# Optimization experiments

Measured on AMD Instinct MI355X. Metric: run time of the kernel, lower is better.

Reference implementation:

```python
import jax, jax.numpy as jnp
import numpy as np

N = 20000          # nodes
E = 320000         # edges
IN_C = 512         # input features
HID = 512          # 2*out_channels (first GCN layer width)
OUT = 256          # out_channels == num_hidden
PROJ = 256         # num_proj_hidden


def _gcn_conv(x, W, b, src, dst):
    """PyG GCNConv: x' = D^{-1/2}(A+I)D^{-1/2} X W + b (self-loops added)."""
    n = x.shape[0]
    x = x @ W  # [N, F_out]
    ones = jnp.ones((src.shape[0],), x.dtype)
    deg = jax.ops.segment_sum(ones, dst, num_segments=n) + 1.0  # +1 self-loop
    dis = jax.lax.rsqrt(deg)
    coef = dis[src] * dis[dst]                      # [E]
    agg = jax.ops.segment_sum(x[src] * coef[:, None], dst, num_segments=n)
    agg = agg + x * (dis * dis)[:, None]            # self-loop messages
    return agg + b


def setup_inputs() -> dict:
    key = jax.random.key(0)
    ks = jax.random.split(key, 12)
    s = 0.02
    return {
        "node_features": jax.random.normal(ks[0], (N, IN_C), jnp.float32),
        "edge_index": jax.random.randint(ks[1], (2, E), 0, N, jnp.int64),
        "W1": jax.random.normal(ks[2], (IN_C, HID), jnp.float32) * s,
        "b1": jnp.zeros((HID,), jnp.float32),
        "W2": jax.random.normal(ks[3], (HID, OUT), jnp.float32) * s,
        "b2": jnp.zeros((OUT,), jnp.float32),
        "a": jnp.asarray(0.25, jnp.float32),  # shared PReLU weight
        "W3": jax.random.normal(ks[4], (OUT, PROJ), jnp.float32) * s,
        "b3": jnp.zeros((PROJ,), jnp.float32),
        "W4": jax.random.normal(ks[5], (PROJ, OUT), jnp.float32) * s,
        "b4": jnp.zeros((OUT,), jnp.float32),
    }


def reference(node_features, edge_index, W1, b1, W2, b2, a, W3, b3, W4, b4):
    src, dst = edge_index[0], edge_index[1]
    prelu = lambda x: jnp.where(x > 0, x, a * x)
    h = prelu(_gcn_conv(node_features, W1, b1, src, dst))
    h = prelu(_gcn_conv(h, W2, b2, src, dst))
    # projection MLP: Linear -> ELU -> Linear
    h2 = jax.nn.elu(h @ W3 + b3)
    return h2 @ W4 + b4
```

## Files before the change

kernel.cpp:

```cpp
#include <hip/hip_runtime.h>

typedef unsigned short u16;
typedef unsigned int   u32;
typedef __attribute__((ext_vector_type(8))) short short8;
typedef __attribute__((ext_vector_type(4))) float f32x4;

__device__ __forceinline__ float bf2f(u16 h){
    return __uint_as_float(((u32)h) << 16);
}
__device__ __forceinline__ u16 f2bf(float f){
    u32 u = __float_as_uint(f);
    u += 0x7fffu + ((u >> 16) & 1u);
    return (u16)(u >> 16);
}

__global__ void probe_all(const u16* __restrict__ w1, const int* __restrict__ ei,
                          const void* b1, const void* b2, const void* b3,
                          const void* b4, const void* av,
                          int* __restrict__ f32f, int* __restrict__ efmt,
                          int* __restrict__ zf,
                          u16* d1, u16* d2, u16* d3, u16* d4, u16* da){
    __shared__ int sf32, sfmt;
    int t = threadIdx.x;
    if (t == 0){ sf32 = 0; sfmt = 0; }
    __syncthreads();
    {
        int huge = 0;
        #pragma unroll
        for (int k = 0; k < 16; k++){
            u16 h = w1[t * 16 + k];
            if (((h >> 7) & 0xFF) >= 0x7F) huge = 1;
        }
        if (huge) atomicOr(&sf32, 1);
    }
    if (ei[2*t + 1] != 0) atomicOr(&sfmt, 1);
    __syncthreads();
    int f32 = sf32, fmt = sfmt;
    if (t == 0){ f32f[0] = f32; efmt[0] = fmt; zf[0] = 0; }
    #define CV(s,i) (f32 ? f2bf(((const float*)(s))[i]) : ((const u16*)(s))[i])
    d1[t]       = CV(b1, t);
    d1[t + 256] = CV(b1, t + 256);
    d2[t] = CV(b2, t);
    d3[t] = CV(b3, t);
    d4[t] = CV(b4, t);
    if (t == 0) da[0] = CV(av, 0);
    #undef CV
}

__device__ __forceinline__ int eload(const int* ei, int fmt, int idx){
    return fmt ? ei[idx] : ei[2*idx];
}

__global__ void deg_count(const int* __restrict__ ei, const int* __restrict__ efmt,
                          int* __restrict__ cnt, int E, int N){
    int e = blockIdx.x * 256 + threadIdx.x;
    if (e < E){
        int d = eload(ei, efmt[0], E + e);
        if ((unsigned)d < (unsigned)N) atomicAdd(&cnt[d], 1);
    }
}

__global__ void scan1(const int* __restrict__ cnt, int* __restrict__ incl,
                      int* __restrict__ bsum, int N){
    __shared__ int s[256];
    int t = threadIdx.x, i = blockIdx.x * 256 + t;
    int v = (i < N) ? cnt[i] : 0;
    s[t] = v;
    __syncthreads();
    #pragma unroll
    for (int off = 1; off < 256; off <<= 1){
        int u = (t >= off) ? s[t - off] : 0;
        __syncthreads();
        s[t] += u;
        __syncthreads();
    }
    if (i < N) incl[i] = s[t];
    if (t == 255) bsum[blockIdx.x] = s[255];
}

__global__ void scan2(const int* __restrict__ bsum, int* __restrict__ boff,
                      int nb, int* __restrict__ rowstart_last){
    __shared__ int s[128];
    int t = threadIdx.x;
    int v = (t < nb) ? bsum[t] : 0;
    s[t] = v;
    __syncthreads();
    #pragma unroll
    for (int off = 1; off < 128; off <<= 1){
        int u = (t >= off) ? s[t - off] : 0;
        __syncthreads();
        s[t] += u;
        __syncthreads();
    }
    if (t < nb) boff[t] = s[t] - v;
    if (t == nb - 1) rowstart_last[0] = s[t];
}

__global__ void scan3(const int* __restrict__ cnt, const int* __restrict__ incl,
                      const int* __restrict__ boff, int* __restrict__ rowstart,
                      int* __restrict__ cursor, float* __restrict__ dis, int N){
    int i = blockIdx.x * 256 + threadIdx.x;
    if (i < N){
        int v = cnt[i];
        int rsv = boff[blockIdx.x] + incl[i] - v;
        rowstart[i] = rsv;
        cursor[i]   = rsv;
        dis[i] = rsqrtf((float)v + 1.0f);
    }
}

__global__ void csr_fill(const int* __restrict__ ei, const int* __restrict__ efmt,
                         int* __restrict__ cursor, int* __restrict__ csr_src,
                         int E, int N){
    int e = blockIdx.x * 256 + threadIdx.x;
    if (e < E){
        int fmt = efmt[0];
        int d = eload(ei, fmt, E + e);
        if ((unsigned)d < (unsigned)N){
            int p = atomicAdd(&cursor[d], 1);
            csr_src[p] = eload(ei, fmt, e);
        }
    }
}

__global__ void transpose_cvt(const void* __restrict__ in, const int* __restrict__ flag,
                              u16* __restrict__ out, int K, int N){
    __shared__ u16 t[32][33];
    int bx = blockIdx.x * 32;
    int by = blockIdx.y * 32;
    int x = threadIdx.x, y = threadIdx.y;
    int f32 = flag[0];
    #pragma unroll
    for (int i = 0; i < 32; i += 8){
        size_t idx = (size_t)(by + y + i) * N + bx + x;
        t[y + i][x] = f32 ? f2bf(((const float*)in)[idx]) : ((const u16*)in)[idx];
    }
    __syncthreads();
    #pragma unroll
    for (int i = 0; i < 32; i += 8)
        out[(size_t)(bx + y + i) * K + by + x] = t[x][y + i];
}

#define TM 64
#define TN 128
#define BK 32
#define BKP 40

template<int MODE, int OUTF>
__global__ __launch_bounds__(256) void gemm_mfma(
    const void* __restrict__ A, const int* __restrict__ af32,
    const u16* __restrict__ BT,
    const u16* __restrict__ bias, void* __restrict__ Cv,
    int M, int K, int N)
{
    __shared__ __align__(16) u16 As[TM * BKP];
    __shared__ __align__(16) u16 Bs[TN * BKP];
    int tid  = threadIdx.x;
    int lane = tid & 63;
    int wave = tid >> 6;
    int waveM = wave >> 1, waveN = wave & 1;
    int bm = blockIdx.x * TM;
    int bn = blockIdx.y * TN;
    int f32 = af32[0];

    f32x4 acc[2][4] = {};

    int alr = tid >> 2;
    int alc = (tid & 3) * 8;
    int blr = tid >> 1;
    int blc = (tid & 1) * 16;

    for (int k0 = 0; k0 < K; k0 += BK){
        {
            int gr = bm + alr;
            short8 v = {0,0,0,0,0,0,0,0};
            if (gr < M){
                if (f32){
                    const float* p = (const float*)A + (size_t)gr * K + k0 + alc;
                    f32x4 a0 = *(const f32x4*)p;
                    f32x4 a1 = *(const f32x4*)(p + 4);
                    #pragma unroll
                    for (int j = 0; j < 4; j++){
                        v[j]   = (short)f2bf(a0[j]);
                        v[4+j] = (short)f2bf(a1[j]);
                    }
                } else {
                    v = *(const short8*)((const u16*)A + (size_t)gr * K + k0 + alc);
                }
            }
            *(short8*)&As[alr * BKP + alc] = v;
        }
        {
            const u16* p = BT + (size_t)(bn + blr) * K + k0 + blc;
            short8 v0 = *(const short8*)p;
            short8 v1 = *(const short8*)(p + 8);
            *(short8*)&Bs[blr * BKP + blc]     = v0;
            *(short8*)&Bs[blr * BKP + blc + 8] = v1;
        }
        __syncthreads();
        int q = lane >> 4;
        int r16 = lane & 15;
        short8 af[2], bfr[4];
        #pragma unroll
        for (int i = 0; i < 2; i++)
            af[i]  = *(const short8*)&As[(waveM*32 + i*16 + r16) * BKP + q*8];
        #pragma unroll
        for (int j = 0; j < 4; j++)
            bfr[j] = *(const short8*)&Bs[(waveN*64 + j*16 + r16) * BKP + q*8];
        #pragma unroll
        for (int i = 0; i < 2; i++)
            #pragma unroll
            for (int j = 0; j < 4; j++)
                acc[i][j] = __builtin_amdgcn_mfma_f32_16x16x32_bf16(af[i], bfr[j], acc[i][j], 0, 0, 0);
        __syncthreads();
    }

    int q = lane >> 4;
    int c16 = lane & 15;
    #pragma unroll
    for (int i = 0; i < 2; i++){
        #pragma unroll
        for (int j = 0; j < 4; j++){
            int gcol = bn + waveN*64 + j*16 + c16;
            float bvv = (MODE >= 1) ? bf2f(bias[gcol]) : 0.f;
            #pragma unroll
            for (int r = 0; r < 4; r++){
                int grow = bm + waveM*32 + i*16 + q*4 + r;
                if (grow < M){
                    float v = acc[i][j][r] + bvv;
                    if (MODE == 2) v = (v > 0.f) ? v : expm1f(v);
                    if (OUTF) ((float*)Cv)[(size_t)grow * N + gcol] = v;
                    else      ((u16*)Cv)[(size_t)grow * N + gcol] = f2bf(v);
                }
            }
        }
    }
}

template<int F, int NPB>
__global__ __launch_bounds__(F/8*NPB) void aggregate(
    const u16* __restrict__ XW, const int* __restrict__ rowstart,
    const int* __restrict__ csr_src, const float* __restrict__ dis,
    const u16* __restrict__ bias, const u16* __restrict__ aptr,
    u16* __restrict__ out, int N)
{
    int node = blockIdx.x * NPB + threadIdx.y;
    if (node >= N) return;
    int tf = threadIdx.x * 8;
    float a  = bf2f(aptr[0]);
    float di = dis[node];
    int e0 = rowstart[node], e1 = rowstart[node + 1];
    float acc[8] = {0,0,0,0,0,0,0,0};
    int e = e0;
    for (; e + 8 <= e1; e += 8){
        int   si[8];
        float ci[8];
        short8 vi[8];
        #pragma unroll
        for (int u = 0; u < 8; u++) si[u] = csr_src[e + u];
        #pragma unroll
        for (int u = 0; u < 8; u++) ci[u] = dis[si[u]];
        #pragma unroll
        for (int u = 0; u < 8; u++)
            vi[u] = *(const short8*)(XW + (size_t)si[u] * F + tf);
        #pragma unroll
        for (int u = 0; u < 8; u++)
            #pragma unroll
            for (int j = 0; j < 8; j++)
                acc[j] += ci[u] * bf2f((u16)vi[u][j]);
    }
    for (; e + 4 <= e1; e += 4){
        int s0 = csr_src[e], s1 = csr_src[e+1], s2 = csr_src[e+2], s3 = csr_src[e+3];
        float c0 = dis[s0], c1 = dis[s1], c2 = dis[s2], c3 = dis[s3];
        short8 v0 = *(const short8*)(XW + (size_t)s0 * F + tf);
        short8 v1 = *(const short8*)(XW + (size_t)s1 * F + tf);
        short8 v2 = *(const short8*)(XW + (size_t)s2 * F + tf);
        short8 v3 = *(const short8*)(XW + (size_t)s3 * F + tf);
        #pragma unroll
        for (int j = 0; j < 8; j++)
            acc[j] += c0*bf2f((u16)v0[j]) + c1*bf2f((u16)v1[j])
                    + c2*bf2f((u16)v2[j]) + c3*bf2f((u16)v3[j]);
    }
    for (; e < e1; e++){
        int s = csr_src[e];
        float c = dis[s];
        short8 v = *(const short8*)(XW + (size_t)s * F + tf);
        #pragma unroll
        for (int j = 0; j < 8; j++) acc[j] += c * bf2f((u16)v[j]);
    }
    {
        short8 v = *(const short8*)(XW + (size_t)node * F + tf);
        #pragma unroll
        for (int j = 0; j < 8; j++) acc[j] += di * bf2f((u16)v[j]);
    }
    short8 bv = *(const short8*)(bias + tf);
    short8 o;
    #pragma unroll
    for (int j = 0; j < 8; j++){
        float x = di * acc[j] + bf2f((u16)bv[j]);
        x = (x > 0.f) ? x : a * x;
        o[j] = (short)f2bf(x);
    }
    *(short8*)(out + (size_t)node * F + tf) = o;
}

extern "C" void kernel_launch(void* const* d_in, const int* in_sizes, int n_in,
                              void* d_out, int out_size, void* d_ws, size_t ws_size,
                              hipStream_t stream)
{
    int iX=0, iEI=1, iW1=2, ib1=3, iW2=4, ib2=5, ia=6, iW3=7, ib3=8, iW4=9, ib4=10;
    {
        int jX=-1,jEI=-1,jW1=-1,jb1=-1,jW2=-1,ja=-1,jW3=-1,jW4=-1,jb2=-1,jb3=-1,jb4=-1;
        int n64k=0, n256=0;
        for (int i = 0; i < n_in; i++){
            switch (in_sizes[i]){
                case 10240000: jX = i; break;
                case 640000:   jEI = i; break;
                case 262144:   jW1 = i; break;
                case 131072:   jW2 = i; break;
                case 512:      jb1 = i; break;
                case 1:        ja = i; break;
                case 65536:    if (n64k++ == 0) jW3 = i; else jW4 = i; break;
                case 256: {
                    int k = n256++;
                    if (k == 0) jb2 = i; else if (k == 1) jb3 = i; else jb4 = i;
                } break;
                default: break;
            }
        }
        if (jX>=0&&jEI>=0&&jW1>=0&&jb1>=0&&jW2>=0&&ja>=0&&jW3>=0&&jW4>=0&&jb2>=0&&jb3>=0&&jb4>=0){
            iX=jX; iEI=jEI; iW1=jW1; ib1=jb1; iW2=jW2; ib2=jb2; ia=ja; iW3=jW3; ib3=jb3; iW4=jW4; ib4=jb4;
        }
    }
    int N = in_sizes[iX] / 512;
    int E = in_sizes[iEI] / 2;
    const int* EI = (const int*)d_in[iEI];
    float* OUT = (float*)d_out;
    u16*   S   = (u16*)d_out;

    char* ws = (char*)d_ws;
    size_t off = 0;
    auto alloc = [&](size_t bytes)->char*{
        char* p = ws + off;
        off = (off + bytes + 255) & ~(size_t)255;
        return p;
    };
    int nb = (N + 255) / 256;
    int*   cnt  = (int*)  alloc((size_t)N*4);
    int*   incl = (int*)  alloc((size_t)N*4);
    int*   bsum = (int*)  alloc(512);
    int*   boff = (int*)  alloc(512);
    int*   efmt = (int*)  alloc(4);
    int*   f32f = (int*)  alloc(4);
    int*   zf   = (int*)  alloc(4);
    float* dis  = (float*)alloc((size_t)N*4);
    int*   rs   = (int*)  alloc((size_t)(N+1)*4);
    int*   cur  = (int*)  alloc((size_t)N*4);
    int*   csr  = (int*)  alloc((size_t)E*4);
    u16*   WT1  = (u16*)  alloc((size_t)512*512*2);
    u16*   WT2  = (u16*)  alloc((size_t)256*512*2);
    u16*   WT3  = (u16*)  alloc((size_t)256*256*2);
    u16*   WT4  = (u16*)  alloc((size_t)256*256*2);
    u16*   b1c  = (u16*)  alloc((size_t)512*2);
    u16*   b2c  = (u16*)  alloc((size_t)256*2);
    u16*   b3c  = (u16*)  alloc((size_t)256*2);
    u16*   b4c  = (u16*)  alloc((size_t)256*2);
    u16*   ac   = (u16*)  alloc((size_t)8*2);
    u16*   h1   = (u16*)  alloc((size_t)N*512*2);
    u16*   P    = (u16*)  alloc((size_t)N*256*2);

    if (ws_size < off) return;

    hipMemsetAsync(cnt, 0, (size_t)N*4, stream);
    probe_all<<<1, 256, 0, stream>>>((const u16*)d_in[iW1], EI,
                                     d_in[ib1], d_in[ib2], d_in[ib3], d_in[ib4],
                                     d_in[ia], f32f, efmt, zf,
                                     b1c, b2c, b3c, b4c, ac);

    int egrid = (E + 255) / 256;
    deg_count<<<egrid, 256, 0, stream>>>(EI, efmt, cnt, E, N);
    scan1<<<nb, 256, 0, stream>>>(cnt, incl, bsum, N);
    scan2<<<1, 128, 0, stream>>>(bsum, boff, nb, rs + N);
    scan3<<<nb, 256, 0, stream>>>(cnt, incl, boff, rs, cur, dis, N);
    csr_fill<<<egrid, 256, 0, stream>>>(EI, efmt, cur, csr, E, N);

    transpose_cvt<<<dim3(512/32, 512/32), dim3(32,8), 0, stream>>>(d_in[iW1], f32f, WT1, 512, 512);
    transpose_cvt<<<dim3(256/32, 512/32), dim3(32,8), 0, stream>>>(d_in[iW2], f32f, WT2, 512, 256);
    transpose_cvt<<<dim3(256/32, 256/32), dim3(32,8), 0, stream>>>(d_in[iW3], f32f, WT3, 256, 256);
    transpose_cvt<<<dim3(256/32, 256/32), dim3(32,8), 0, stream>>>(d_in[iW4], f32f, WT4, 256, 256);

    int gm = (N + TM - 1) / TM;
    dim3 g512(gm, 512 / TN);
    dim3 g256(gm, 256 / TN);

    gemm_mfma<0,0><<<g512, 256, 0, stream>>>(d_in[iX], f32f, WT1, nullptr, S, N, 512, 512);
    aggregate<512,2><<<(N+1)/2, dim3(64,2), 0, stream>>>(S, rs, csr, dis, b1c, ac, h1, N);

    u16* Q = (u16*)d_out;
    gemm_mfma<0,0><<<g256, 256, 0, stream>>>(h1, zf, WT2, nullptr, P, N, 512, 256);
    aggregate<256,4><<<(N+3)/4, dim3(32,4), 0, stream>>>(P, rs, csr, dis, b2c, ac, Q, N);

    gemm_mfma<2,0><<<g256, 256, 0, stream>>>(Q, zf, WT3, b3c, P, N, 256, 256);
    gemm_mfma<1,1><<<g256, 256, 0, stream>>>(P, zf, WT4, b4c, OUT, N, 256, 256);
}
```

Baseline: 295.7 us.

## Use persistent work-stealing waves for GCN aggregation and merge weight transposes

Replaces the one-block-per-few-nodes aggregation kernels with a persistent grid of 1024 blocks whose 64-lane waves grab groups of 4 nodes from an atomic ticket counter. The intent is to balance the uneven per-node degree and cut block launch overhead. For the 256-wide layer each lane now handles 4 features, so one full wave covers a row. The four weight transpose launches are merged into one 3D-grid launch. The change adds atomic contention on a single counter and serialises the nodes within each wave.

```diff
diff --git a/kernel.cpp b/kernel.cpp
--- a/kernel.cpp
+++ b/kernel.cpp
@@ -3,6 +3,7 @@
 typedef unsigned short u16;
 typedef unsigned int   u32;
 typedef __attribute__((ext_vector_type(8))) short short8;
+typedef __attribute__((ext_vector_type(4))) short short4v;
 typedef __attribute__((ext_vector_type(4))) float f32x4;
 
 __device__ __forceinline__ float bf2f(u16 h){
@@ -18,7 +19,8 @@
                           const void* b1, const void* b2, const void* b3,
                           const void* b4, const void* av,
                           int* __restrict__ f32f, int* __restrict__ efmt,
-                          int* __restrict__ zf,
+                          int* __restrict__ zf, int* __restrict__ tk1,
+                          int* __restrict__ tk2,
                           u16* d1, u16* d2, u16* d3, u16* d4, u16* da){
     __shared__ int sf32, sfmt;
     int t = threadIdx.x;
@@ -36,7 +38,7 @@
     if (ei[2*t + 1] != 0) atomicOr(&sfmt, 1);
     __syncthreads();
     int f32 = sf32, fmt = sfmt;
-    if (t == 0){ f32f[0] = f32; efmt[0] = fmt; zf[0] = 0; }
+    if (t == 0){ f32f[0] = f32; efmt[0] = fmt; zf[0] = 0; tk1[0] = 0; tk2[0] = 0; }
     #define CV(s,i) (f32 ? f2bf(((const float*)(s))[i]) : ((const u16*)(s))[i])
     d1[t]       = CV(b1, t);
     d1[t + 256] = CV(b1, t + 256);
@@ -123,11 +125,20 @@
     }
 }
 
-__global__ void transpose_cvt(const void* __restrict__ in, const int* __restrict__ flag,
-                              u16* __restrict__ out, int K, int N){
-    __shared__ u16 t[32][33];
+__global__ void transpose_all(const void* w1, const void* w2, const void* w3,
+                              const void* w4, const int* __restrict__ flag,
+                              u16* o1, u16* o2, u16* o3, u16* o4){
+    const void* in; u16* out; int K, N;
+    switch (blockIdx.z){
+        case 0:  in = w1; out = o1; K = 512; N = 512; break;
+        case 1:  in = w2; out = o2; K = 512; N = 256; break;
+        case 2:  in = w3; out = o3; K = 256; N = 256; break;
+        default: in = w4; out = o4; K = 256; N = 256; break;
+    }
     int bx = blockIdx.x * 32;
     int by = blockIdx.y * 32;
+    if (bx >= N || by >= K) return;
+    __shared__ u16 t[32][33];
     int x = threadIdx.x, y = threadIdx.y;
     int f32 = flag[0];
     #pragma unroll
@@ -237,71 +248,85 @@
     }
 }
 
-template<int F, int NPB>
-__global__ __launch_bounds__(F/8*NPB) void aggregate(
+template<int F> struct AggVec;
+template<> struct AggVec<512>{ using T = short8;  enum{ EPL = 8 }; };
+template<> struct AggVec<256>{ using T = short4v; enum{ EPL = 4 }; };
+
+template<int F>
+__global__ __launch_bounds__(256) void aggregate_ws(
     const u16* __restrict__ XW, const int* __restrict__ rowstart,
     const int* __restrict__ csr_src, const float* __restrict__ dis,
     const u16* __restrict__ bias, const u16* __restrict__ aptr,
-    u16* __restrict__ out, int N)
+    u16* __restrict__ out, int N, int* __restrict__ ticket)
 {
-    int node = blockIdx.x * NPB + threadIdx.y;
-    if (node >= N) return;
-    int tf = threadIdx.x * 8;
-    float a  = bf2f(aptr[0]);
-    float di = dis[node];
-    int e0 = rowstart[node], e1 = rowstart[node + 1];
-    float acc[8] = {0,0,0,0,0,0,0,0};
-    int e = e0;
-    for (; e + 8 <= e1; e += 8){
-        int   si[8];
-        float ci[8];
-        short8 vi[8];
-        #pragma unroll
-        for (int u = 0; u < 8; u++) si[u] = csr_src[e + u];
-        #pragma unroll
-        for (int u = 0; u < 8; u++) ci[u] = dis[si[u]];
-        #pragma unroll
-        for (int u = 0; u < 8; u++)
-            vi[u] = *(const short8*)(XW + (size_t)si[u] * F + tf);
-        #pragma unroll
-        for (int u = 0; u < 8; u++)
+    using V = typename AggVec<F>::T;
+    constexpr int EPL = AggVec<F>::EPL;
+    int lane = threadIdx.x & 63;
+    int tf = lane * EPL;
+    float a = bf2f(aptr[0]);
+    for (;;){
+        int base = 0;
+        if (lane == 0) base = atomicAdd(ticket, 4);
+        base = __shfl(base, 0, 64);
+        if (base >= N) return;
+        int nend = (base + 4 < N) ? base + 4 : N;
+        for (int node = base; node < nend; node++){
+            float di = dis[node];
+            int e0 = rowstart[node], e1 = rowstart[node + 1];
+            float acc[EPL];
             #pragma unroll
-            for (int j = 0; j < 8; j++)
-                acc[j] += ci[u] * bf2f((u16)vi[u][j]);
-    }
-    for (; e + 4 <= e1; e += 4){
-        int s0 = csr_src[e], s1 = csr_src[e+1], s2 = csr_src[e+2], s3 = csr_src[e+3];
-        float c0 = dis[s0], c1 = dis[s1], c2 = dis[s2], c3 = dis[s3];
-        short8 v0 = *(const short8*)(XW + (size_t)s0 * F + tf);
-        short8 v1 = *(const short8*)(XW + (size_t)s1 * F + tf);
-        short8 v2 = *(const short8*)(XW + (size_t)s2 * F + tf);
-        short8 v3 = *(const short8*)(XW + (size_t)s3 * F + tf);
-        #pragma unroll
-        for (int j = 0; j < 8; j++)
-            acc[j] += c0*bf2f((u16)v0[j]) + c1*bf2f((u16)v1[j])
-                    + c2*bf2f((u16)v2[j]) + c3*bf2f((u16)v3[j]);
-    }
-    for (; e < e1; e++){
-        int s = csr_src[e];
-        float c = dis[s];
-        short8 v = *(const short8*)(XW + (size_t)s * F + tf);
-        #pragma unroll
-        for (int j = 0; j < 8; j++) acc[j] += c * bf2f((u16)v[j]);
-    }
-    {
-        short8 v = *(const short8*)(XW + (size_t)node * F + tf);
-        #pragma unroll
-        for (int j = 0; j < 8; j++) acc[j] += di * bf2f((u16)v[j]);
-    }
-    short8 bv = *(const short8*)(bias + tf);
-    short8 o;
-    #pragma unroll
-    for (int j = 0; j < 8; j++){
-        float x = di * acc[j] + bf2f((u16)bv[j]);
-        x = (x > 0.f) ? x : a * x;
-        o[j] = (short)f2bf(x);
-    }
-    *(short8*)(out + (size_t)node * F + tf) = o;
+            for (int j = 0; j < EPL; j++) acc[j] = 0.f;
+            int e = e0;
+            for (; e + 8 <= e1; e += 8){
+                int si[8]; float ci[8]; V vi[8];
+                #pragma unroll
+                for (int u = 0; u < 8; u++) si[u] = csr_src[e + u];
+                #pragma unroll
+                for (int u = 0; u < 8; u++) ci[u] = dis[si[u]];
+                #pragma unroll
+                for (int u = 0; u < 8; u++)
+                    vi[u] = *(const V*)(XW + (size_t)si[u] * F + tf);
+                #pragma unroll
+                for (int u = 0; u < 8; u++)
+                    #pragma unroll
+                    for (int j = 0; j < EPL; j++)
+                        acc[j] += ci[u] * bf2f((u16)vi[u][j]);
+            }
+            for (; e + 4 <= e1; e += 4){
+                int s0 = csr_src[e], s1 = csr_src[e+1], s2 = csr_src[e+2], s3 = csr_src[e+3];
+                float c0 = dis[s0], c1 = dis[s1], c2 = dis[s2], c3 = dis[s3];
+                V v0 = *(const V*)(XW + (size_t)s0 * F + tf);
+                V v1 = *(const V*)(XW + (size_t)s1 * F + tf);
+                V v2 = *(const V*)(XW + (size_t)s2 * F + tf);
+                V v3 = *(const V*)(XW + (size_t)s3 * F + tf);
+                #pragma unroll
+                for (int j = 0; j < EPL; j++)
+                    acc[j] += c0*bf2f((u16)v0[j]) + c1*bf2f((u16)v1[j])
+                            + c2*bf2f((u16)v2[j]) + c3*bf2f((u16)v3[j]);
+            }
+            for (; e < e1; e++){
+                int s = csr_src[e];
+                float c = dis[s];
+                V v = *(const V*)(XW + (size_t)s * F + tf);
+                #pragma unroll
+                for (int j = 0; j < EPL; j++) acc[j] += c * bf2f((u16)v[j]);
+            }
+            {
+                V v = *(const V*)(XW + (size_t)node * F + tf);
+                #pragma unroll
+                for (int j = 0; j < EPL; j++) acc[j] += di * bf2f((u16)v[j]);
+            }
+            V bv = *(const V*)(bias + tf);
+            V o;
+            #pragma unroll
+            for (int j = 0; j < EPL; j++){
+                float x = di * acc[j] + bf2f((u16)bv[j]);
+                x = (x > 0.f) ? x : a * x;
+                o[j] = (short)f2bf(x);
+            }
+            *(V*)(out + (size_t)node * F + tf) = o;
+        }
+    }
 }
 
 extern "C" void kernel_launch(void* const* d_in, const int* in_sizes, int n_in,
@@ -353,6 +378,8 @@
     int*   efmt = (int*)  alloc(4);
     int*   f32f = (int*)  alloc(4);
     int*   zf   = (int*)  alloc(4);
+    int*   tk1  = (int*)  alloc(4);
+    int*   tk2  = (int*)  alloc(4);
     float* dis  = (float*)alloc((size_t)N*4);
     int*   rs   = (int*)  alloc((size_t)(N+1)*4);
     int*   cur  = (int*)  alloc((size_t)N*4);
@@ -374,7 +401,7 @@
     hipMemsetAsync(cnt, 0, (size_t)N*4, stream);
     probe_all<<<1, 256, 0, stream>>>((const u16*)d_in[iW1], EI,
                                      d_in[ib1], d_in[ib2], d_in[ib3], d_in[ib4],
-                                     d_in[ia], f32f, efmt, zf,
+                                     d_in[ia], f32f, efmt, zf, tk1, tk2,
                                      b1c, b2c, b3c, b4c, ac);
 
     int egrid = (E + 255) / 256;
@@ -384,21 +411,20 @@
     scan3<<<nb, 256, 0, stream>>>(cnt, incl, boff, rs, cur, dis, N);
     csr_fill<<<egrid, 256, 0, stream>>>(EI, efmt, cur, csr, E, N);
 
-    transpose_cvt<<<dim3(512/32, 512/32), dim3(32,8), 0, stream>>>(d_in[iW1], f32f, WT1, 512, 512);
-    transpose_cvt<<<dim3(256/32, 512/32), dim3(32,8), 0, stream>>>(d_in[iW2], f32f, WT2, 512, 256);
-    transpose_cvt<<<dim3(256/32, 256/32), dim3(32,8), 0, stream>>>(d_in[iW3], f32f, WT3, 256, 256);
-    transpose_cvt<<<dim3(256/32, 256/32), dim3(32,8), 0, stream>>>(d_in[iW4], f32f, WT4, 256, 256);
+    transpose_all<<<dim3(16, 16, 4), dim3(32, 8), 0, stream>>>(
+        d_in[iW1], d_in[iW2], d_in[iW3], d_in[iW4], f32f, WT1, WT2, WT3, WT4);
 
     int gm = (N + TM - 1) / TM;
     dim3 g512(gm, 512 / TN);
     dim3 g256(gm, 256 / TN);
+    int agrid = 1024;
 
     gemm_mfma<0,0><<<g512, 256, 0, stream>>>(d_in[iX], f32f, WT1, nullptr, S, N, 512, 512);
-    aggregate<512,2><<<(N+1)/2, dim3(64,2), 0, stream>>>(S, rs, csr, dis, b1c, ac, h1, N);
+    aggregate_ws<512><<<agrid, 256, 0, stream>>>(S, rs, csr, dis, b1c, ac, h1, N, tk1);
 
     u16* Q = (u16*)d_out;
     gemm_mfma<0,0><<<g256, 256, 0, stream>>>(h1, zf, WT2, nullptr, P, N, 512, 256);
-    aggregate<256,4><<<(N+3)/4, dim3(32,4), 0, stream>>>(P, rs, csr, dis, b2c, ac, Q, N);
+    aggregate_ws<256><<<agrid, 256, 0, stream>>>(P, rs, csr, dis, b2c, ac, Q, N, tk2);
 
     gemm_mfma<2,0><<<g256, 256, 0, stream>>>(Q, zf, WT3, b3c, P, N, 256, 256);
     gemm_mfma<1,1><<<g256, 256, 0, stream>>>(P, zf, WT4, b4c, OUT, N, 256, 256);
```

Result: slower. 471.5 us (+59.4%).
